# Kernel tuning notes

Hardware: AMD Instinct MI355X
Metric: run time of the kernel (lower is better)

Reference implementation:

```python
import jax, jax.numpy as jnp
import numpy as np

VERY_SMOL_NUM = -1e9  # undefined global in source; interpreted as large negative mask value
D_K = 128


def setup_inputs() -> dict:
    key = jax.random.key(0)
    k1, k2, k3 = jax.random.split(key, 3)
    B, S, D = 16, 2048, D_K
    Q = jax.random.normal(k1, (B, S, D), dtype=jnp.float32)
    K = jax.random.normal(k2, (B, S, D), dtype=jnp.float32)
    V = jax.random.normal(k3, (B, S, D), dtype=jnp.float32)
    return {"Q": Q, "K": K, "V": V}


def reference(Q, K, V):
    B, S, d_k = Q.shape
    # scores: [B, S, S] = Q @ K^T, scaled by 1/sqrt(d_k)
    x = jnp.einsum("bqd,bkd->bqk", Q, K) / jnp.sqrt(jnp.asarray(d_k, Q.dtype))
    # mask() is called unconditionally in the source (masked=False -> applied once):
    # add strict upper-triangular VERY_SMOL_NUM
    tri = jnp.triu(jnp.ones((S, S), dtype=x.dtype), k=1) * jnp.asarray(VERY_SMOL_NUM, x.dtype)
    x = x + tri  # broadcasts over batch, matching torch.triu on full shape
    # Softmax over dim=1 (query axis), as in the source (torch.nn.Softmax(dim=1))
    x = jax.nn.softmax(x, axis=1)
    return jnp.einsum("bqk,bkd->bqd", x, V)
```

## Files before the change

kernel.cpp:

```cpp
#include <hip/hip_runtime.h>


#define B_ 16
#define S_ 2048
#define D_ 128
#define QSCALE 0.12751744416825963f
#define NEG_BIG -1e30f
#define NCH 16
#define CHQ 128
#define PB 2162688

#define ROWW 136

#define LDS_BARRIER()                                  \
  do {                                                 \
    asm volatile("s_waitcnt lgkmcnt(0)" ::: "memory"); \
    __builtin_amdgcn_s_barrier();                      \
    __builtin_amdgcn_sched_barrier(0);                 \
  } while (0)

typedef short bf16x8 __attribute__((ext_vector_type(8)));
typedef float f32x4 __attribute__((ext_vector_type(4)));
typedef unsigned short u16x4 __attribute__((ext_vector_type(4)));
typedef unsigned int u32x2 __attribute__((ext_vector_type(2)));

#if defined(__has_builtin)
#if __has_builtin(__builtin_amdgcn_exp2f)
#define EXP2F(x) __builtin_amdgcn_exp2f(x)
#endif
#endif
#ifndef EXP2F
extern "C" __device__ float __ocml_exp2_f32(float);
#define EXP2F(x) __ocml_exp2_f32(x)
#endif

static __device__ __forceinline__ unsigned short f2bf(float f) {
  unsigned int u = __builtin_bit_cast(unsigned int, f);
  u += 0x7FFFu + ((u >> 16) & 1u);
  return (unsigned short)(u >> 16);
}

__global__ __launch_bounds__(256) void sdpa_convert(
    const float* __restrict__ Qr, const float* __restrict__ Kr,
    unsigned short* __restrict__ Qb, unsigned short* __restrict__ Kb) {
  const size_t t = (size_t)blockIdx.x * 256 + threadIdx.x;
  const float* src = blockIdx.y ? Kr : Qr;
  unsigned short* dstp = blockIdx.y ? Kb : Qb;
  const float sc = blockIdx.y ? 1.0f : QSCALE;
  f32x4 x = ((const f32x4*)src)[t];
  u16x4 o;
#pragma unroll
  for (int j = 0; j < 4; ++j) o[j] = f2bf(x[j] * sc);
  ((u16x4*)dstp)[t] = o;
}

__global__ __launch_bounds__(256, 4) void sdpa_pass1(
    const short* __restrict__ Qb, const short* __restrict__ Kb,
    float* __restrict__ lp_ws, unsigned short* __restrict__ Pt) {
  const int bid = blockIdx.x;
  int j = bid >> 4;
  int g = 0;
  while (j >= NCH - g) {
    j -= NCH - g;
    ++g;
  }
  const int ci = g + j;
  const int b = (bid & 7) + 8 * ((bid >> 3) & 1);

  __shared__ __align__(16) short Qst[2][32 * ROWW];
  const int tid = threadIdx.x;
  const int w = tid >> 6, lane = tid & 63, quad = lane >> 4, l15 = lane & 15;
  const int gg = 2 * g + (w >> 1);
  const int gb = 64 * gg;
  const int kb = gb + (w & 1) * 32;

  const size_t koff = ((size_t)b * S_ + kb + l15) * D_ + quad * 8;
  bf16x8 kh0[4], kh1[4];
#pragma unroll
  for (int c = 0; c < 4; ++c) {
    kh0[c] = *(const bf16x8*)(Kb + koff + c * 32);
    kh1[c] = *(const bf16x8*)(Kb + koff + 16 * D_ + c * 32);
  }

  const int nrp = S_ - gb;
  const size_t grp =
      (size_t)4 * ((size_t)gg * S_ - (size_t)(32 * gg) * (gg - 1));
  unsigned short* pw0 = Pt + (size_t)b * PB +
                        16 * (grp + (size_t)(2 * (w & 1)) * nrp) + quad * 4;
  unsigned short* pw1 = pw0 + (size_t)16 * nrp;

  const int sr = tid >> 3, sseg = tid & 7;
  const int q_start = CHQ * ci;

  {
    const short* sq = Qb + ((size_t)(b * S_ + q_start + sr)) * D_ + sseg * 16;
    bf16x8 h0 = *(const bf16x8*)(sq), h1 = *(const bf16x8*)(sq + 8);
    short* dst = &Qst[0][sr * ROWW + sseg * 16];
    *(bf16x8*)(dst) = h0;
    *(bf16x8*)(dst + 8) = h1;
  }
  LDS_BARRIER();

#define EMIT(q0s_, ktb_, cA_, pw_, lp_)                                       \
  do {                                                                        \
    float s0_ = cA_[0], s1_ = cA_[1], s2_ = cA_[2], s3_ = cA_[3];             \
    if ((q0s_) < (ktb_) + 16) {              \
      const int q_ = (q0s_) + l15;                                            \
      if ((ktb_) + quad * 4 + 0 > q_) s0_ = NEG_BIG;                          \
      if ((ktb_) + quad * 4 + 1 > q_) s1_ = NEG_BIG;                          \
      if ((ktb_) + quad * 4 + 2 > q_) s2_ = NEG_BIG;                          \
      if ((ktb_) + quad * 4 + 3 > q_) s3_ = NEG_BIG;                          \
    }                                                                         \
    const float e0_ = EXP2F(s0_), e1_ = EXP2F(s1_);                           \
    const float e2_ = EXP2F(s2_), e3_ = EXP2F(s3_);                           \
    lp_[0] += e0_;                                                            \
    lp_[1] += e1_;                                                            \
    lp_[2] += e2_;                                                            \
    lp_[3] += e3_;                                                            \
    unsigned int w0_, w1_;                                                    \
    asm("v_cvt_pk_bf16_f32 %0, %1, %2" : "=v"(w0_) : "v"(e0_), "v"(e1_));     \
    asm("v_cvt_pk_bf16_f32 %0, %1, %2" : "=v"(w1_) : "v"(e2_), "v"(e3_));     \
    u32x2 pk2_ = {w0_, w1_};                                                  \
    *(u32x2*)((pw_) + (size_t)((q0s_)-gb + l15) * 16) = pk2_;                 \
  } while (0)

  f32x4 lp0 = {0.f, 0.f, 0.f, 0.f}, lp1 = {0.f, 0.f, 0.f, 0.f};
#pragma unroll
  for (int it = 0; it < 4; ++it) {
    const int q0 = q_start + it * 32;
    const int cur = it & 1;
    bf16x8 h0, h1;
    if (it < 3) {
      const short* sq =
          Qb + ((size_t)(b * S_ + q0 + 32 + sr)) * D_ + sseg * 16;
      h0 = *(const bf16x8*)(sq);
      h1 = *(const bf16x8*)(sq + 8);
    }
#pragma unroll
    for (int sub = 0; sub < 2; ++sub) {
      const int q0s = q0 + sub * 16;
      if (q0s >= gb) {
        const short* rowp = &Qst[cur][(sub * 16 + l15) * ROWW + quad * 8];
        bf16x8 q0v = *(const bf16x8*)(rowp);
        bf16x8 q1v = *(const bf16x8*)(rowp + 32);
        bf16x8 q2v = *(const bf16x8*)(rowp + 64);
        bf16x8 q3v = *(const bf16x8*)(rowp + 96);
        f32x4 c0 = {0.f, 0.f, 0.f, 0.f};
        f32x4 c1 = {0.f, 0.f, 0.f, 0.f};
        c0 = __builtin_amdgcn_mfma_f32_16x16x32_bf16(kh0[0], q0v, c0, 0, 0, 0);
        c1 = __builtin_amdgcn_mfma_f32_16x16x32_bf16(kh1[0], q0v, c1, 0, 0, 0);
        c0 = __builtin_amdgcn_mfma_f32_16x16x32_bf16(kh0[1], q1v, c0, 0, 0, 0);
        c1 = __builtin_amdgcn_mfma_f32_16x16x32_bf16(kh1[1], q1v, c1, 0, 0, 0);
        c0 = __builtin_amdgcn_mfma_f32_16x16x32_bf16(kh0[2], q2v, c0, 0, 0, 0);
        c1 = __builtin_amdgcn_mfma_f32_16x16x32_bf16(kh1[2], q2v, c1, 0, 0, 0);
        c0 = __builtin_amdgcn_mfma_f32_16x16x32_bf16(kh0[3], q3v, c0, 0, 0, 0);
        c1 = __builtin_amdgcn_mfma_f32_16x16x32_bf16(kh1[3], q3v, c1, 0, 0, 0);
        EMIT(q0s, kb, c0, pw0, lp0);
        EMIT(q0s, kb + 16, c1, pw1, lp1);
      }
    }
    if (it < 3) {
      short* dst = &Qst[1 - cur][sr * ROWW + sseg * 16];
      *(bf16x8*)(dst) = h0;
      *(bf16x8*)(dst + 8) = h1;
    }
    LDS_BARRIER();
  }
#undef EMIT

#pragma unroll
  for (int d = 1; d < 16; d <<= 1) {
#pragma unroll
    for (int r = 0; r < 4; ++r) {
      lp0[r] += __shfl_xor(lp0[r], d, 64);
      lp1[r] += __shfl_xor(lp1[r], d, 64);
    }
  }
  if (l15 == 0) {
    float* dst = lp_ws + ((size_t)b * NCH + ci) * S_ + kb;
    *(f32x4*)(dst + quad * 4) = lp0;
    *(f32x4*)(dst + 16 + quad * 4) = lp1;
  }
}

__global__ __launch_bounds__(256) void sdpa_vscale(
    const float* __restrict__ Vr, const float* __restrict__ lp_ws,
    unsigned short* __restrict__ Vf) {
  __shared__ float Vld[32][132];
  __shared__ float as[32];
  const int kt = blockIdx.x, b = blockIdx.y, tid = threadIdx.x;
  const int k0 = kt * 32;
  const int row = tid >> 3, seg = tid & 7;
  const float* src = Vr + ((size_t)(b * S_ + k0 + row)) * D_ + seg * 16;
#pragma unroll
  for (int j = 0; j < 4; ++j) {
    f32x4 x = *(const f32x4*)(src + 4 * j);
    *(f32x4*)&Vld[row][seg * 16 + 4 * j] = x;
  }
  if (tid < 32) {
    const int k = k0 + tid;
    const int first = k >> 7;
    float l = 0.f;
#pragma unroll
    for (int ci = 0; ci < NCH; ++ci)
      if (ci >= first) l += lp_ws[((size_t)b * NCH + ci) * S_ + k];
    as[tid] = 1.0f / l;
  }
  __syncthreads();
  unsigned short* dst = Vf + ((size_t)(b * 64 + kt)) * 4096 + (size_t)tid * 16;
#pragma unroll
  for (int i = 0; i < 2; ++i) {
    const int u = tid * 2 + i;
    const int dt = u >> 6, l15 = (u >> 2) & 15, quad = u & 3;
    bf16x8 o;
#pragma unroll
    for (int e = 0; e < 8; ++e) {
      const int k = quad * 8 + e;
      o[e] = (short)f2bf(Vld[k][dt * 16 + l15] * as[k]);
    }
    *(bf16x8*)(dst + i * 8) = o;
  }
}

__global__ __launch_bounds__(256, 2) void sdpa_pass2(
    const unsigned short* __restrict__ Pt,
    const unsigned short* __restrict__ Vf, float* __restrict__ Out) {
  const int bid = blockIdx.x;
  const int b = (bid & 7) + 8 * ((bid >> 3) & 1);
  const int jj = bid >> 4;
  const int dh = jj & 1;
  const int py = jj >> 1;
  const int tid = threadIdx.x;
  const int w = tid >> 6, lane = tid & 63, quad = lane >> 4, l15 = lane & 15;

  const unsigned short* Pb = Pt + (size_t)b * PB + (quad & 1) * 8;
  const unsigned short* Vbase = Vf + (size_t)b * 64 * 4096 +
                                (size_t)(dh * 4) * 512 + l15 * 32 + quad * 8;
  const int qsel = quad >> 1;

#define LOADT(tp_, A0_, A1_, V_)                                             \
  do {                                                                       \
    const int nr_ = S_ - 64 * (tp_);                                         \
    const int pitch_ = 16 * nr_;                                             \
    const unsigned short* p0_ =                                              \
        Pb + 2048 * (tp_) * (65 - (tp_)) + qsel * pitch_ +                   \
        (qwl - 64 * (tp_)) * 16;                                             \
    A0_ = *(const bf16x8*)p0_;                                               \
    A1_ = *(const bf16x8*)(p0_ + 2 * pitch_);                                \
    const unsigned short* v0_ = Vbase + (size_t)(2 * (tp_)) * 4096;          \
    _Pragma("unroll") for (int d_ = 0; d_ < 4; ++d_) {                       \
      V_[d_] = *(const bf16x8*)(v0_ + d_ * 512);                             \
      V_[d_ + 4] = *(const bf16x8*)(v0_ + 4096 + d_ * 512);                  \
    }                                                                        \
  } while (0)

#define MMAT(A0_, A1_, V_)                                                   \
  do {                                                                       \
    _Pragma("unroll") for (int d_ = 0; d_ < 4; ++d_) acc[d_] =               \
        __builtin_amdgcn_mfma_f32_16x16x32_bf16(A0_, V_[d_], acc[d_], 0, 0,  \
                                                0);                          \
    _Pragma("unroll") for (int d_ = 0; d_ < 4; ++d_) acc[d_] =               \
        __builtin_amdgcn_mfma_f32_16x16x32_bf16(A1_, V_[d_ + 4], acc[d_], 0, \
                                                0, 0);                       \
  } while (0)

#pragma unroll
  for (int ti = 0; ti < 2; ++ti) {
    const int bx = ti ? (31 - py) : py;
    const int qw = 64 * bx + 16 * w;
    const int qwl = qw + l15;
    const int count = bx + 1;

    f32x4 acc[4];
#pragma unroll
    for (int d = 0; d < 4; ++d) acc[d] = (f32x4){0.f, 0.f, 0.f, 0.f};

    bf16x8 xA0, xA1, xV[8], yA0, yA1, yV[8], zA0, zA1, zV[8];
    LOADT(0, xA0, xA1, xV);
    if (count > 1) LOADT(1, yA0, yA1, yV);
    if (count > 2) LOADT(2, zA0, zA1, zV);
    int t = 0;
    for (; t + 3 <= count; t += 3) {
      MMAT(xA0, xA1, xV);
      if (t + 3 < count) LOADT(t + 3, xA0, xA1, xV);
      MMAT(yA0, yA1, yV);
      if (t + 4 < count) LOADT(t + 4, yA0, yA1, yV);
      MMAT(zA0, zA1, zV);
      if (t + 5 < count) LOADT(t + 5, zA0, zA1, zV);
    }
    if (t < count) MMAT(xA0, xA1, xV);
    if (t + 1 < count) MMAT(yA0, yA1, yV);

#pragma unroll
    for (int r = 0; r < 4; ++r) {
      float* op =
          Out + ((size_t)b * S_ + qw + quad * 4 + r) * D_ + dh * 64 + l15;
#pragma unroll
      for (int d = 0; d < 4; ++d) op[d * 16] = acc[d][r];
    }
  }
#undef LOADT
#undef MMAT
}

extern "C" void kernel_launch(void* const* d_in, const int* in_sizes, int n_in,
                              void* d_out, int out_size, void* d_ws,
                              size_t ws_size, hipStream_t stream) {
  char* wsp = (char*)d_ws;
  float* lp_ws = (float*)wsp;
  char* p = wsp + (2 << 20);
  const size_t TSZ = (size_t)B_ * S_ * D_ * 2;
  unsigned short* Qb = (unsigned short*)(p);
  unsigned short* Kb = (unsigned short*)(p + TSZ);
  unsigned short* Vf = (unsigned short*)(p + 2 * TSZ);
  unsigned short* Pt = (unsigned short*)(p + 3 * TSZ);

  sdpa_convert<<<dim3((B_ * S_ * D_ / 4) / 256, 2), 256, 0, stream>>>(
      (const float*)d_in[0], (const float*)d_in[1], Qb, Kb);
  sdpa_pass1<<<dim3(NCH * 136), 256, 0, stream>>>(
      (const short*)Qb, (const short*)Kb, lp_ws, Pt);
  sdpa_vscale<<<dim3(S_ / 32, B_), 256, 0, stream>>>((const float*)d_in[2],
                                                     lp_ws, Vf);
  sdpa_pass2<<<dim3(512), 256, 0, stream>>>(Pt, Vf, (float*)d_out);
}
```

Before: 153.3 us.

## Split pass2 key range across two blocks with atomic accumulation

Pass2 now splits each output tile's key-tile range into two halves handled by separate blocks, doubling the grid to 1024 blocks and raising launch bounds occupancy to 4. Partial results are combined with atomic adds into an output buffer zeroed by a new memset. The goal is better load balance and more parallelism on the 256-CU device. The cost is atomic traffic, an extra memset launch, and nondeterministic summation order. It also drops the sched_barrier from the LDS barrier macro.

```diff
diff --git a/kernel.cpp b/kernel.cpp
--- a/kernel.cpp
+++ b/kernel.cpp
@@ -16,7 +16,6 @@
   do {                                                 \
     asm volatile("s_waitcnt lgkmcnt(0)" ::: "memory"); \
     __builtin_amdgcn_s_barrier();                      \
-    __builtin_amdgcn_sched_barrier(0);                 \
   } while (0)
 
 typedef short bf16x8 __attribute__((ext_vector_type(8)));
@@ -222,14 +221,15 @@
   }
 }
 
-__global__ __launch_bounds__(256, 2) void sdpa_pass2(
+__global__ __launch_bounds__(256, 4) void sdpa_pass2(
     const unsigned short* __restrict__ Pt,
     const unsigned short* __restrict__ Vf, float* __restrict__ Out) {
   const int bid = blockIdx.x;
   const int b = (bid & 7) + 8 * ((bid >> 3) & 1);
   const int jj = bid >> 4;
-  const int dh = jj & 1;
-  const int py = jj >> 1;
+  const int kh = jj & 1;
+  const int dh = (jj >> 1) & 1;
+  const int py = jj >> 2;
   const int tid = threadIdx.x;
   const int w = tid >> 6, lane = tid & 63, quad = lane >> 4, l15 = lane & 15;
 
@@ -270,33 +270,44 @@
     const int qw = 64 * bx + 16 * w;
     const int qwl = qw + l15;
     const int count = bx + 1;
-
-    f32x4 acc[4];
-#pragma unroll
-    for (int d = 0; d < 4; ++d) acc[d] = (f32x4){0.f, 0.f, 0.f, 0.f};
-
-    bf16x8 xA0, xA1, xV[8], yA0, yA1, yV[8], zA0, zA1, zV[8];
-    LOADT(0, xA0, xA1, xV);
-    if (count > 1) LOADT(1, yA0, yA1, yV);
-    if (count > 2) LOADT(2, zA0, zA1, zV);
-    int t = 0;
-    for (; t + 3 <= count; t += 3) {
-      MMAT(xA0, xA1, xV);
-      if (t + 3 < count) LOADT(t + 3, xA0, xA1, xV);
-      MMAT(yA0, yA1, yV);
-      if (t + 4 < count) LOADT(t + 4, yA0, yA1, yV);
-      MMAT(zA0, zA1, zV);
-      if (t + 5 < count) LOADT(t + 5, zA0, zA1, zV);
-    }
-    if (t < count) MMAT(xA0, xA1, xV);
-    if (t + 1 < count) MMAT(yA0, yA1, yV);
-
-#pragma unroll
-    for (int r = 0; r < 4; ++r) {
-      float* op =
-          Out + ((size_t)b * S_ + qw + quad * 4 + r) * D_ + dh * 64 + l15;
-#pragma unroll
-      for (int d = 0; d < 4; ++d) op[d * 16] = acc[d][r];
+    const int lo = (count * kh) >> 1;
+    const int hi = (count * (kh + 1)) >> 1;
+    const int n = hi - lo;
+    if (n > 0) {
+      f32x4 acc[4];
+#pragma unroll
+      for (int d = 0; d < 4; ++d) acc[d] = (f32x4){0.f, 0.f, 0.f, 0.f};
+
+      bf16x8 xA0, xA1, xV[8], yA0, yA1, yV[8];
+      LOADT(lo, xA0, xA1, xV);
+      if (n > 1) LOADT(lo + 1, yA0, yA1, yV);
+      int t = lo;
+      while (t + 3 < hi) {
+        MMAT(xA0, xA1, xV);
+        LOADT(t + 2, xA0, xA1, xV);
+        MMAT(yA0, yA1, yV);
+        LOADT(t + 3, yA0, yA1, yV);
+        t += 2;
+      }
+      if (t + 2 < hi) {
+        MMAT(xA0, xA1, xV);
+        LOADT(t + 2, xA0, xA1, xV);
+        MMAT(yA0, yA1, yV);
+        MMAT(xA0, xA1, xV);
+      } else if (t + 1 < hi) {
+        MMAT(xA0, xA1, xV);
+        MMAT(yA0, yA1, yV);
+      } else {
+        MMAT(xA0, xA1, xV);
+      }
+
+#pragma unroll
+      for (int r = 0; r < 4; ++r) {
+        float* op =
+            Out + ((size_t)b * S_ + qw + quad * 4 + r) * D_ + dh * 64 + l15;
+#pragma unroll
+        for (int d = 0; d < 4; ++d) unsafeAtomicAdd(op + d * 16, acc[d][r]);
+      }
     }
   }
 #undef LOADT
@@ -315,11 +326,12 @@
   unsigned short* Vf = (unsigned short*)(p + 2 * TSZ);
   unsigned short* Pt = (unsigned short*)(p + 3 * TSZ);
 
+  hipMemsetAsync(d_out, 0, out_size, stream);
   sdpa_convert<<<dim3((B_ * S_ * D_ / 4) / 256, 2), 256, 0, stream>>>(
       (const float*)d_in[0], (const float*)d_in[1], Qb, Kb);
   sdpa_pass1<<<dim3(NCH * 136), 256, 0, stream>>>(
       (const short*)Qb, (const short*)Kb, lp_ws, Pt);
   sdpa_vscale<<<dim3(S_ / 32, B_), 256, 0, stream>>>((const float*)d_in[2],
                                                      lp_ws, Vf);
-  sdpa_pass2<<<dim3(512), 256, 0, stream>>>(Pt, Vf, (float*)d_out);
-}
+  sdpa_pass2<<<dim3(1024), 256, 0, stream>>>(Pt, Vf, (float*)d_out);
+}
```

Result: slower. 169.0 us (+10.2%).

## Split pass2 over key chunks with atomic accumulation and larger per-wave tiles

Applied to the files above, without the earlier changes.

The P·V kernel is restructured so that each block handles a 128-query tile and a quarter of its key range (split-K). Each wave computes a 64x64 output tile, which raises reuse of the loaded V fragments across four row sub-tiles. Partial results are combined with atomic float adds into an output that is zeroed by an added memset. The intent is better load balance across the causal triangle and fewer redundant V loads, at the cost of atomic traffic, an extra memset, and higher register pressure. A sched_barrier is also removed from the LDS barrier macro.

```diff
diff --git a/kernel.cpp b/kernel.cpp
--- a/kernel.cpp
+++ b/kernel.cpp
@@ -16,7 +16,6 @@
   do {                                                 \
     asm volatile("s_waitcnt lgkmcnt(0)" ::: "memory"); \
     __builtin_amdgcn_s_barrier();                      \
-    __builtin_amdgcn_sched_barrier(0);                 \
   } while (0)
 
 typedef short bf16x8 __attribute__((ext_vector_type(8)));
@@ -228,79 +227,76 @@
   const int bid = blockIdx.x;
   const int b = (bid & 7) + 8 * ((bid >> 3) & 1);
   const int jj = bid >> 4;
-  const int dh = jj & 1;
-  const int py = jj >> 1;
+  const int ks = jj & 3;
+  const int py = jj >> 2;
   const int tid = threadIdx.x;
   const int w = tid >> 6, lane = tid & 63, quad = lane >> 4, l15 = lane & 15;
+  const int qh = w & 1;
+  const int dhw = w >> 1;
 
   const unsigned short* Pb = Pt + (size_t)b * PB + (quad & 1) * 8;
   const unsigned short* Vbase = Vf + (size_t)b * 64 * 4096 +
-                                (size_t)(dh * 4) * 512 + l15 * 32 + quad * 8;
+                                (size_t)(dhw * 4) * 512 + l15 * 32 + quad * 8;
   const int qsel = quad >> 1;
 
-#define LOADT(tp_, A0_, A1_, V_)                                             \
-  do {                                                                       \
-    const int nr_ = S_ - 64 * (tp_);                                         \
-    const int pitch_ = 16 * nr_;                                             \
-    const unsigned short* p0_ =                                              \
-        Pb + 2048 * (tp_) * (65 - (tp_)) + qsel * pitch_ +                   \
-        (qwl - 64 * (tp_)) * 16;                                             \
-    A0_ = *(const bf16x8*)p0_;                                               \
-    A1_ = *(const bf16x8*)(p0_ + 2 * pitch_);                                \
-    const unsigned short* v0_ = Vbase + (size_t)(2 * (tp_)) * 4096;          \
-    _Pragma("unroll") for (int d_ = 0; d_ < 4; ++d_) {                       \
-      V_[d_] = *(const bf16x8*)(v0_ + d_ * 512);                             \
-      V_[d_ + 4] = *(const bf16x8*)(v0_ + 4096 + d_ * 512);                  \
-    }                                                                        \
-  } while (0)
-
-#define MMAT(A0_, A1_, V_)                                                   \
-  do {                                                                       \
-    _Pragma("unroll") for (int d_ = 0; d_ < 4; ++d_) acc[d_] =               \
-        __builtin_amdgcn_mfma_f32_16x16x32_bf16(A0_, V_[d_], acc[d_], 0, 0,  \
-                                                0);                          \
-    _Pragma("unroll") for (int d_ = 0; d_ < 4; ++d_) acc[d_] =               \
-        __builtin_amdgcn_mfma_f32_16x16x32_bf16(A1_, V_[d_ + 4], acc[d_], 0, \
-                                                0, 0);                       \
-  } while (0)
-
 #pragma unroll
   for (int ti = 0; ti < 2; ++ti) {
-    const int bx = ti ? (31 - py) : py;
-    const int qw = 64 * bx + 16 * w;
-    const int qwl = qw + l15;
-    const int count = bx + 1;
-
-    f32x4 acc[4];
-#pragma unroll
-    for (int d = 0; d < 4; ++d) acc[d] = (f32x4){0.f, 0.f, 0.f, 0.f};
-
-    bf16x8 xA0, xA1, xV[8], yA0, yA1, yV[8], zA0, zA1, zV[8];
-    LOADT(0, xA0, xA1, xV);
-    if (count > 1) LOADT(1, yA0, yA1, yV);
-    if (count > 2) LOADT(2, zA0, zA1, zV);
-    int t = 0;
-    for (; t + 3 <= count; t += 3) {
-      MMAT(xA0, xA1, xV);
-      if (t + 3 < count) LOADT(t + 3, xA0, xA1, xV);
-      MMAT(yA0, yA1, yV);
-      if (t + 4 < count) LOADT(t + 4, yA0, yA1, yV);
-      MMAT(zA0, zA1, zV);
-      if (t + 5 < count) LOADT(t + 5, zA0, zA1, zV);
-    }
-    if (t < count) MMAT(xA0, xA1, xV);
-    if (t + 1 < count) MMAT(yA0, yA1, yV);
-
-#pragma unroll
-    for (int r = 0; r < 4; ++r) {
-      float* op =
-          Out + ((size_t)b * S_ + qw + quad * 4 + r) * D_ + dh * 64 + l15;
-#pragma unroll
-      for (int d = 0; d < 4; ++d) op[d * 16] = acc[d][r];
-    }
-  }
-#undef LOADT
-#undef MMAT
+    const int t = ti ? (15 - py) : py;
+    const int count = 2 * t + 2;
+    const int lo = (count * ks) >> 2;
+    int hi = (count * (ks + 1)) >> 2;
+    if (!qh) hi = min(hi, count - 1);
+    if (hi > lo) {
+      const int qbase = 128 * t + 64 * qh;
+      f32x4 acc[4][4];
+#pragma unroll
+      for (int r = 0; r < 4; ++r)
+#pragma unroll
+        for (int d = 0; d < 4; ++d) acc[r][d] = (f32x4){0.f, 0.f, 0.f, 0.f};
+
+      for (int tp = lo; tp < hi; ++tp) {
+        const int pitch = 16 * (S_ - 64 * tp);
+        const unsigned short* pg = Pb + 2048 * tp * (65 - tp) + qsel * pitch +
+                                   (qbase + l15 - 64 * tp) * 16;
+        bf16x8 A0[4], A1[4];
+#pragma unroll
+        for (int r = 0; r < 4; ++r) {
+          A0[r] = *(const bf16x8*)(pg + r * 256);
+          A1[r] = *(const bf16x8*)(pg + r * 256 + 2 * pitch);
+        }
+        const unsigned short* v0 = Vbase + (size_t)(2 * tp) * 4096;
+        bf16x8 V0[4], V1[4];
+#pragma unroll
+        for (int d = 0; d < 4; ++d) {
+          V0[d] = *(const bf16x8*)(v0 + d * 512);
+          V1[d] = *(const bf16x8*)(v0 + 4096 + d * 512);
+        }
+#pragma unroll
+        for (int r = 0; r < 4; ++r)
+#pragma unroll
+          for (int d = 0; d < 4; ++d)
+            acc[r][d] = __builtin_amdgcn_mfma_f32_16x16x32_bf16(
+                A0[r], V0[d], acc[r][d], 0, 0, 0);
+#pragma unroll
+        for (int r = 0; r < 4; ++r)
+#pragma unroll
+          for (int d = 0; d < 4; ++d)
+            acc[r][d] = __builtin_amdgcn_mfma_f32_16x16x32_bf16(
+                A1[r], V1[d], acc[r][d], 0, 0, 0);
+      }
+#pragma unroll
+      for (int r = 0; r < 4; ++r)
+#pragma unroll
+        for (int rr = 0; rr < 4; ++rr) {
+          float* op = Out +
+                      ((size_t)b * S_ + qbase + 16 * r + quad * 4 + rr) * D_ +
+                      dhw * 64 + l15;
+#pragma unroll
+          for (int d = 0; d < 4; ++d)
+            unsafeAtomicAdd(op + d * 16, acc[r][d][rr]);
+        }
+    }
+  }
 }
 
 extern "C" void kernel_launch(void* const* d_in, const int* in_sizes, int n_in,
@@ -315,6 +311,7 @@
   unsigned short* Vf = (unsigned short*)(p + 2 * TSZ);
   unsigned short* Pt = (unsigned short*)(p + 3 * TSZ);
 
+  hipMemsetAsync(d_out, 0, out_size, stream);
   sdpa_convert<<<dim3((B_ * S_ * D_ / 4) / 256, 2), 256, 0, stream>>>(
       (const float*)d_in[0], (const float*)d_in[1], Qb, Kb);
   sdpa_pass1<<<dim3(NCH * 136), 256, 0, stream>>>(
```

After: 183.4 us. 1.2x slower.
